# Kernel tuning notes

Measured on AMD Instinct MI355X. Metric: run time of the kernel, lower is better.

Reference implementation:

```python
import jax, jax.numpy as jnp
import numpy as np
from itertools import permutations

S_SPK, B, T, C = 2, 16, 300, 3000
NUM_STATES, NUM_ARCS = 400, 1200
DEN_STATES, DEN_ARCS = 3000, 60000
DEN_SCALE = 1.0
NEG = -1e30


def setup_inputs() -> dict:
    key = jax.random.key(0)
    ks = jax.random.split(key, 14)
    est_llhs = jax.nn.log_softmax(
        jax.random.normal(ks[0], (S_SPK, B, T, C), jnp.float32), axis=-1)
    seqlengths = jax.random.randint(ks[1], (B,), T // 2, T + 1, jnp.int32)
    num_src = jax.random.randint(ks[2], (S_SPK, B, NUM_ARCS), 0, NUM_STATES, jnp.int32)
    num_dst = jax.random.randint(ks[3], (S_SPK, B, NUM_ARCS), 0, NUM_STATES, jnp.int32)
    num_label = jax.random.randint(ks[4], (S_SPK, B, NUM_ARCS), 0, C, jnp.int32)
    num_weight = -2.0 * jax.random.uniform(ks[5], (S_SPK, B, NUM_ARCS), jnp.float32)
    num_start = -5.0 * jax.random.uniform(ks[6], (S_SPK, B, NUM_STATES), jnp.float32)
    num_final = -5.0 * jax.random.uniform(ks[7], (S_SPK, B, NUM_STATES), jnp.float32)
    den_src = jax.random.randint(ks[8], (DEN_ARCS,), 0, DEN_STATES, jnp.int32)
    den_dst = jax.random.randint(ks[9], (DEN_ARCS,), 0, DEN_STATES, jnp.int32)
    den_label = jax.random.randint(ks[10], (DEN_ARCS,), 0, C, jnp.int32)
    den_weight = -2.0 * jax.random.uniform(ks[11], (DEN_ARCS,), jnp.float32)
    den_start = -5.0 * jax.random.uniform(ks[12], (DEN_STATES,), jnp.float32)
    den_final = -5.0 * jax.random.uniform(ks[13], (DEN_STATES,), jnp.float32)
    return dict(est_llhs=est_llhs, seqlengths=seqlengths,
                num_src=num_src, num_dst=num_dst, num_label=num_label,
                num_weight=num_weight, num_start=num_start, num_final=num_final,
                den_src=den_src, den_dst=den_dst, den_label=den_label,
                den_weight=den_weight, den_start=den_start, den_final=den_final)


def _segment_lse(scores, idx, n):
    # stable log-sum-exp scatter over destination states
    m = jax.ops.segment_max(scores, idx, num_segments=n)
    m_safe = jnp.where(jnp.isfinite(m), m, 0.0)
    s = jax.ops.segment_sum(jnp.exp(scores - m_safe[idx]), idx, num_segments=n)
    s_safe = jnp.where(s > 0, s, 1.0)
    return jnp.where(s > 0, m_safe + jnp.log(s_safe), NEG)


def _fsa_logZ(llh, seqlen, src, dst, lab, w, start, final):
    # forward algorithm: alpha_{t+1}[dst] = LSE_arcs(alpha_t[src] + w + llh[t, lab])
    n = start.shape[0]
    mask = jnp.arange(llh.shape[0]) < seqlen

    def step(alpha, inp):
        t_llh, valid = inp
        scores = alpha[src] + w + t_llh[lab]
        new_alpha = _segment_lse(scores, dst, n)
        return jnp.where(valid, new_alpha, alpha), None

    alpha, _ = jax.lax.scan(step, start, (llh, mask))
    return jax.scipy.special.logsumexp(alpha + final)


_num_logZ = jax.vmap(_fsa_logZ)  # all graph args batched over B
_den_logZ = jax.vmap(_fsa_logZ, in_axes=(0, 0, None, None, None, None, None, None))


def reference(est_llhs, seqlengths, num_src, num_dst, num_label, num_weight,
              num_start, num_final, den_src, den_dst, den_label, den_weight,
              den_start, den_final):
    n_spk = est_llhs.shape[0]
    bsz = est_llhs.shape[1]
    # denominator log-marginal per (batch, speaker): [B, S]
    den_llh = jnp.stack(
        [_den_logZ(est_llhs[s], seqlengths, den_src, den_dst, den_label,
                   den_weight, den_start, den_final) for s in range(n_spk)], axis=1)
    # numerator log-marginals for every permutation: [P, B, S]
    perms = list(permutations(range(n_spk)))
    num_llh_perms = jnp.stack([
        jnp.stack([_num_logZ(est_llhs[s], seqlengths, num_src[p], num_dst[p],
                             num_label[p], num_weight[p], num_start[p], num_final[p])
                   for s, p in enumerate(perm)], axis=1)
        for perm in perms], axis=0)
    # best permutation per utterance
    idxs = jnp.argmax(num_llh_perms.sum(axis=2), axis=0)  # [B]
    num_llh = jnp.take_along_axis(
        num_llh_perms, jnp.broadcast_to(idxs[None, :, None], (1, bsz, n_spk)),
        axis=0)[0]  # [B, S]
    loss = -(num_llh - DEN_SCALE * den_llh)
    return loss.sum()
```

## Files before the change

kernel.cpp:

```cpp
#include <hip/hip_runtime.h>
#include <hip/hip_bf16.h>

#define S_SPK 2
#define BATCH 16
#define TMAX 300
#define CLASSES 3000
#define NUM_STATES 400
#define NUM_ARCS 1200
#define DEN_STATES 3000
#define DEN_ARCS 60000

#define BLK 768
#define NWAVE 12
#define KCH 4
#define CHST 750
#define NSEQ 32
#define NUM_CAP_G 2400
#define NGRAPH 32

#define WS_DEN_ARCS   0
#define WS_NUM_ARCS   576000
#define WS_DEN_CNT    1190400
#define WS_DEN_R      1202400
#define WS_DEN_CUR    1214416
#define WS_NUM_CNT    1226416
#define WS_NUM_R      1277616
#define WS_NUM_CUR    1328944
#define WS_GALPHA     1380144
#define WS_FLAGS      2148144
#define WS_BINS       2156336
#define WS_DEN_Z      2156592
#define WS_NUM_Z      2156720
#define WS_BINCUR     2156976
#define WS_PI         2157232
#define WS_INV        2169232
#define WS_CNTP       2181232
#define WS_ZERO_INTS  (2156592 / 4)

__global__ void zero_ws(int* __restrict__ p, int n) {
    int i = blockIdx.x * blockDim.x + threadIdx.x;
    for (; i < n; i += gridDim.x * blockDim.x) p[i] = 0;
}

__global__ void hist_den(const int* __restrict__ dst, int* __restrict__ cnt) {
    int i = blockIdx.x * blockDim.x + threadIdx.x;
    if (i < DEN_ARCS) atomicAdd(&cnt[dst[i]], 1);
}

__global__ void hist_num(const int* __restrict__ dst, int* __restrict__ cnt) {
    int i = blockIdx.x * blockDim.x + threadIdx.x;
    if (i < NGRAPH * NUM_ARCS) {
        int g = i / NUM_ARCS;
        atomicAdd(&cnt[g * NUM_STATES + dst[i]], 1);
    }
}

__global__ void bin_hist(const int* __restrict__ cnt, int* __restrict__ bins) {
    int s = blockIdx.x * blockDim.x + threadIdx.x;
    if (s < DEN_STATES) {
        int c = cnt[s]; if (c > 63) c = 63;
        atomicAdd(&bins[c], 1);
    }
}

__global__ void bin_scan(const int* __restrict__ bins, int* __restrict__ bincur) {
    __shared__ int sb[64];
    int tid = threadIdx.x;
    sb[tid] = bins[tid];
    __syncthreads();
    int sum = 0;
    for (int b = 63; b > tid; --b) sum += sb[b];
    bincur[tid] = sum;
}

__global__ void rank_scatter(const int* __restrict__ cnt, int* __restrict__ bincur,
                             int* __restrict__ pi, int* __restrict__ inv) {
    int s = blockIdx.x * blockDim.x + threadIdx.x;
    if (s < DEN_STATES) {
        int c = cnt[s]; if (c > 63) c = 63;
        int rank = atomicAdd(&bincur[c], 1);
        int pos = (rank & (KCH - 1)) * CHST + (rank >> 2);
        pi[s] = pos;
        inv[pos] = s;
    }
}

__global__ void permute_cnt(const int* __restrict__ cnt, const int* __restrict__ inv,
                            int* __restrict__ cntp) {
    int p = blockIdx.x * blockDim.x + threadIdx.x;
    if (p < DEN_STATES) cntp[p] = cnt[inv[p]];
}

__global__ void scan_den(const int* __restrict__ cnt, int* __restrict__ R) {
    __shared__ int sc[1024];
    int tid = threadIdx.x;
    int c0 = 0, c1 = 0, c2 = 0, p0 = 0, p1 = 0, p2 = 0, pg = 0;
    if (tid < 1000) {
        c0 = cnt[3 * tid]; c1 = cnt[3 * tid + 1]; c2 = cnt[3 * tid + 2];
        p0 = (c0 + 3) & ~3; p1 = (c1 + 3) & ~3; p2 = (c2 + 3) & ~3;
        pg = p0 + p1 + p2;
    }
    sc[tid] = pg; __syncthreads();
    for (int o = 1; o < 1024; o <<= 1) {
        int v = (tid >= o) ? sc[tid - o] : 0;
        __syncthreads(); sc[tid] += v; __syncthreads();
    }
    int ex = sc[tid] - pg;
    if (tid < 1000) {
        R[3 * tid] = ex; R[3 * tid + 1] = ex + p0; R[3 * tid + 2] = ex + p0 + p1;
    }
    if (tid == 1000) R[3000] = ex;
}

__global__ void scan_num(const int* __restrict__ cnt, int* __restrict__ R) {
    __shared__ int sc[512];
    int g = blockIdx.x, tid = threadIdx.x;
    int c = 0, pg = 0;
    if (tid < NUM_STATES) { c = cnt[g * NUM_STATES + tid]; pg = (c + 3) & ~3; }
    sc[tid] = pg; __syncthreads();
    for (int o = 1; o < 512; o <<= 1) {
        int v = (tid >= o) ? sc[tid - o] : 0;
        __syncthreads(); sc[tid] += v; __syncthreads();
    }
    int ex = sc[tid] - pg;
    if (tid <= NUM_STATES) R[g * (NUM_STATES + 1) + tid] = ex;
}

__global__ void scat_den(const int* __restrict__ src, const int* __restrict__ dst,
                         const int* __restrict__ lab, const float* __restrict__ w,
                         const int* __restrict__ R, int* __restrict__ cur,
                         const int* __restrict__ pi, int2* __restrict__ out) {
    int i = blockIdx.x * blockDim.x + threadIdx.x;
    if (i >= DEN_ARCS) return;
    int dpos = pi[dst[i]];
    int spos = pi[src[i]];
    int pos = R[dpos] + atomicAdd(&cur[dpos], 1);
    out[pos] = make_int2(spos | (lab[i] << 16), __float_as_int(__expf(w[i])));
}

__global__ void scat_num(const int* __restrict__ src, const int* __restrict__ dst,
                         const int* __restrict__ lab, const float* __restrict__ w,
                         const int* __restrict__ R, int* __restrict__ cur,
                         int2* __restrict__ out) {
    int i = blockIdx.x * blockDim.x + threadIdx.x;
    if (i >= NGRAPH * NUM_ARCS) return;
    int g = i / NUM_ARCS;
    int d = dst[i];
    int pos = R[g * (NUM_STATES + 1) + d] + atomicAdd(&cur[g * NUM_STATES + d], 1);
    out[g * NUM_CAP_G + pos] =
        make_int2(src[i] | (lab[i] << 16), __float_as_int(__expf(w[i])));
}

__device__ __forceinline__ void num_fwd(
    const int* __restrict__ R, const int2* __restrict__ arcs,
    const float* __restrict__ start, const float* __restrict__ fin,
    const float* __restrict__ est, int L, float* __restrict__ out,
    float* A0, float* A1, float* p, float* red)
{
    const int tid = threadIdx.x, lane = tid & 63, wid = tid >> 6;

    if (tid < NUM_STATES) A0[tid] = __expf(start[tid]);

    int rs = 0, re = 0;
    if (tid < NUM_STATES) { rs = R[tid]; re = R[tid + 1]; }

    float l0 = est[tid], l1 = est[tid + 768], l2 = est[tid + 1536];
    float l3 = (tid < 696) ? est[tid + 2304] : 0.f;

    float c = 1.f, OFF = 0.f, pend = 0.f;
    const int4* arcs4 = (const int4*)arcs;

    for (int t = 0; t < L; ++t) {
        OFF += pend;
        p[tid] = __expf(l0) * c;        p[tid + 768] = __expf(l1) * c;
        p[tid + 1536] = __expf(l2) * c;
        if (tid < 696) p[tid + 2304] = __expf(l3) * c;
        {
            const float* nr = est + (size_t)((t + 1 < L) ? (t + 1) : t) * CLASSES;
            l0 = nr[tid]; l1 = nr[tid + 768]; l2 = nr[tid + 1536];
            if (tid < 696) l3 = nr[tid + 2304];
        }
        __syncthreads();

        const float* Ac = (t & 1) ? A1 : A0;
        float*       An = (t & 1) ? A0 : A1;
        float a0 = 0.f;
        for (int r = rs; r < re; r += 4) {
            int4 q0 = arcs4[(r >> 1)];
            int4 q1 = arcs4[(r >> 1) + 1];
            a0 += Ac[q0.x & 0xffff] * p[((unsigned)q0.x) >> 16] * __int_as_float(q0.y);
            a0 += Ac[q0.z & 0xffff] * p[((unsigned)q0.z) >> 16] * __int_as_float(q0.w);
            a0 += Ac[q1.x & 0xffff] * p[((unsigned)q1.x) >> 16] * __int_as_float(q1.y);
            a0 += Ac[q1.z & 0xffff] * p[((unsigned)q1.z) >> 16] * __int_as_float(q1.w);
        }
        float mymax = 0.f;
        if (tid < NUM_STATES) { An[tid] = a0; mymax = a0; }
        #pragma unroll
        for (int o = 32; o > 0; o >>= 1) mymax = fmaxf(mymax, __shfl_down(mymax, o, 64));
        if (lane == 0) red[wid] = mymax;
        __syncthreads();
        float M = red[0];
        #pragma unroll
        for (int k = 1; k < NWAVE; ++k) M = fmaxf(M, red[k]);
        M = fmaxf(M, 1e-37f);
        c = 1.0f / M;
        pend = __logf(M);
    }

    const float* Af = (L & 1) ? A1 : A0;
    float fs = 0.f;
    if (tid < NUM_STATES) fs = Af[tid] * __expf(fin[tid]);
    __syncthreads();
    #pragma unroll
    for (int o = 32; o > 0; o >>= 1) fs += __shfl_down(fs, o, 64);
    if (lane == 0) red[wid] = fs;
    __syncthreads();
    if (tid == 0) {
        float s = 0.f;
        #pragma unroll
        for (int k = 0; k < NWAVE; ++k) s += red[k];
        out[0] = OFF + __logf(s);
    }
}

__global__ __launch_bounds__(BLK) void forward_kernel(
    const float* __restrict__ est, const int* __restrict__ seqlen,
    const int2* __restrict__ den_arcs, const int* __restrict__ den_R,
    const float* __restrict__ den_start, const float* __restrict__ den_final,
    const int* __restrict__ den_inv,
    const int2* __restrict__ num_arcs, const int* __restrict__ num_R,
    const float* __restrict__ num_start, const float* __restrict__ num_final,
    float* __restrict__ galpha,
    float* __restrict__ den_z, float* __restrict__ num_z)
{
    __shared__ float S1[2][DEN_STATES];
    __shared__ float S2[2][CLASSES];
    __shared__ float red[2][16];

    const int blk = blockIdx.x;
    const int tid = threadIdx.x, lane = tid & 63, wid = tid >> 6;

    if (blk < KCH * NSEQ) {
        const int seq = blk & 31;
        const int chunk = blk >> 5;
        const int b = seq & 15;
        const int L = seqlen[b];
        const float* est_base = est + (size_t)seq * TMAX * CLASSES;
        const int base = chunk * CHST;
        unsigned* gaU = (unsigned*)galpha;

        int rs = 0, re = 0;
        if (tid < CHST) { rs = den_R[base + tid]; re = den_R[base + tid + 1]; }
        const int4* arcs4 = (const int4*)den_arcs;
        const int4* ap = arcs4 + (rs >> 1);
        const int n4 = (re - rs) >> 2;

        float l0 = est_base[tid], l1 = est_base[tid + 768], l2 = est_base[tid + 1536];
        float l3 = (tid < 696) ? est_base[tid + 2304] : 0.f;

        float OFF = 0.f;

        for (int t = 0; t < L; ++t) {
            const int cur = t & 1;
            float* S1c = S1[cur];
            float* S2c = S2[cur];

            S2c[tid] = __expf(l0); S2c[tid + 768] = __expf(l1); S2c[tid + 1536] = __expf(l2);
            if (tid < 696) S2c[tid + 2304] = __expf(l3);
            {
                const float* nr = est_base + (size_t)((t + 1 < L) ? (t + 1) : t) * CLASSES;
                l0 = nr[tid]; l1 = nr[tid + 768]; l2 = nr[tid + 1536];
                if (tid < 696) l3 = nr[tid + 2304];
            }

            int4 a0 = ap[0], a1 = ap[1], b0 = ap[2], b1 = ap[3];

            if (t == 0) {
                S1c[tid]        = __expf(den_start[den_inv[tid]]);
                S1c[tid + 768]  = __expf(den_start[den_inv[tid + 768]]);
                S1c[tid + 1536] = __expf(den_start[den_inv[tid + 1536]]);
                if (tid < 696) S1c[tid + 2304] = __expf(den_start[den_inv[tid + 2304]]);
            } else {
                const unsigned tg = (unsigned)((t - 1) % 3) + 1u;
                const unsigned* gp = gaU + ((size_t)seq * 2 + ((t - 1) & 1)) * DEN_STATES;
                unsigned u0, u1, u2, u3 = tg;
                for (;;) {
                    u0 = __hip_atomic_load(gp + tid,        __ATOMIC_RELAXED, __HIP_MEMORY_SCOPE_AGENT);
                    u1 = __hip_atomic_load(gp + tid + 768,  __ATOMIC_RELAXED, __HIP_MEMORY_SCOPE_AGENT);
                    u2 = __hip_atomic_load(gp + tid + 1536, __ATOMIC_RELAXED, __HIP_MEMORY_SCOPE_AGENT);
                    if (tid < 696)
                        u3 = __hip_atomic_load(gp + tid + 2304, __ATOMIC_RELAXED, __HIP_MEMORY_SCOPE_AGENT);
                    if ((((u0 & 3u) == tg) && ((u1 & 3u) == tg)) &&
                        (((u2 & 3u) == tg) && ((u3 & 3u) == tg))) break;
                    __builtin_amdgcn_s_sleep(1);
                }
                float x0 = __uint_as_float(u0 & ~3u);
                float x1 = __uint_as_float(u1 & ~3u);
                float x2 = __uint_as_float(u2 & ~3u);
                float x3 = (tid < 696) ? __uint_as_float(u3 & ~3u) : 0.f;
                S1c[tid] = x0; S1c[tid + 768] = x1; S1c[tid + 1536] = x2;
                if (tid < 696) S1c[tid + 2304] = x3;
                float mymax = fmaxf(fmaxf(x0, x1), fmaxf(x2, x3));
                #pragma unroll
                for (int o = 32; o > 0; o >>= 1)
                    mymax = fmaxf(mymax, __shfl_down(mymax, o, 64));
                if (lane == 0) red[cur][wid] = mymax;
            }

            __syncthreads();

            float cM = 1.0f;
            if (t) {
                const float4* r4 = (const float4*)red[cur];
                float4 ra = r4[0], rb = r4[1], rc = r4[2];
                float M = fmaxf(fmaxf(fmaxf(ra.x, ra.y), fmaxf(ra.z, ra.w)),
                         fmaxf(fmaxf(fmaxf(rb.x, rb.y), fmaxf(rb.z, rb.w)),
                               fmaxf(fmaxf(rc.x, rc.y), fmaxf(rc.z, rc.w))));
                M = fmaxf(M, 1e-37f);
                cM = 1.0f / M;
                OFF += __logf(M);
            }

            float acc = 0.f;
            for (int i = 0; i < n4; ++i) {
                int4 p0 = ap[2 * i + 4], p1 = ap[2 * i + 5];
                acc += S1c[a0.x & 0xffff] * S2c[((unsigned)a0.x) >> 16] * __int_as_float(a0.y);
                acc += S1c[a0.z & 0xffff] * S2c[((unsigned)a0.z) >> 16] * __int_as_float(a0.w);
                acc += S1c[a1.x & 0xffff] * S2c[((unsigned)a1.x) >> 16] * __int_as_float(a1.y);
                acc += S1c[a1.z & 0xffff] * S2c[((unsigned)a1.z) >> 16] * __int_as_float(a1.w);
                a0 = b0; a1 = b1; b0 = p0; b1 = p1;
            }

            if (tid < CHST) {
                unsigned uv = (__float_as_uint(acc * cM) & ~3u) | ((unsigned)(t % 3) + 1u);
                __hip_atomic_store(gaU + ((size_t)seq * 2 + cur) * DEN_STATES + base + tid,
                                   uv, __ATOMIC_RELAXED, __HIP_MEMORY_SCOPE_AGENT);
            }
            asm volatile("" ::: "memory");
        }

        if (chunk == 0) {
            __syncthreads();
            const unsigned tg = (unsigned)((L - 1) % 3) + 1u;
            const unsigned* gp = gaU + ((size_t)seq * 2 + ((L - 1) & 1)) * DEN_STATES;
            unsigned u0, u1, u2, u3 = tg;
            for (;;) {
                u0 = __hip_atomic_load(gp + tid,        __ATOMIC_RELAXED, __HIP_MEMORY_SCOPE_AGENT);
                u1 = __hip_atomic_load(gp + tid + 768,  __ATOMIC_RELAXED, __HIP_MEMORY_SCOPE_AGENT);
                u2 = __hip_atomic_load(gp + tid + 1536, __ATOMIC_RELAXED, __HIP_MEMORY_SCOPE_AGENT);
                if (tid < 696)
                    u3 = __hip_atomic_load(gp + tid + 2304, __ATOMIC_RELAXED, __HIP_MEMORY_SCOPE_AGENT);
                if ((((u0 & 3u) == tg) && ((u1 & 3u) == tg)) &&
                    (((u2 & 3u) == tg) && ((u3 & 3u) == tg))) break;
                __builtin_amdgcn_s_sleep(1);
            }
            float fs = __uint_as_float(u0 & ~3u) * __expf(den_final[den_inv[tid]])
                     + __uint_as_float(u1 & ~3u) * __expf(den_final[den_inv[tid + 768]])
                     + __uint_as_float(u2 & ~3u) * __expf(den_final[den_inv[tid + 1536]]);
            if (tid < 696)
                fs += __uint_as_float(u3 & ~3u) * __expf(den_final[den_inv[tid + 2304]]);
            #pragma unroll
            for (int o = 32; o > 0; o >>= 1) fs += __shfl_down(fs, o, 64);
            if (lane == 0) red[0][wid] = fs;
            __syncthreads();
            if (tid == 0) {
                float s = 0.f;
                #pragma unroll
                for (int k = 0; k < NWAVE; ++k) s += red[0][k];
                den_z[seq] = OFF + __logf(s);
            }
        }
    } else {
        const int q = blk - KCH * NSEQ;
        const int b = q & 15;
        const int sp = q >> 4;
        const int s = sp >> 1, pp = sp & 1;
        const int L = seqlen[b];
        const int g = pp * BATCH + b;
        num_fwd(num_R + (size_t)g * (NUM_STATES + 1),
                num_arcs + (size_t)g * NUM_CAP_G,
                num_start + (size_t)g * NUM_STATES,
                num_final + (size_t)g * NUM_STATES,
                est + (size_t)(s * BATCH + b) * TMAX * CLASSES, L, &num_z[q],
                &S1[0][0], &S1[0][1536], &S2[0][0], &red[0][0]);
    }
}

__global__ void loss_kernel(const float* __restrict__ den_z,
                            const float* __restrict__ num_z,
                            float* __restrict__ out)
{
    int tid = threadIdx.x;
    float l = 0.f;
    if (tid < BATCH) {
        int b = tid;
        float z00 = num_z[(0 * 2 + 0) * BATCH + b];
        float z01 = num_z[(0 * 2 + 1) * BATCH + b];
        float z10 = num_z[(1 * 2 + 0) * BATCH + b];
        float z11 = num_z[(1 * 2 + 1) * BATCH + b];
        float perm0 = z00 + z11;
        float perm1 = z01 + z10;
        float n0, n1;
        if (perm0 >= perm1) { n0 = z00; n1 = z11; }
        else                { n0 = z01; n1 = z10; }
        l = -(n0 - den_z[0 * BATCH + b]) - (n1 - den_z[1 * BATCH + b]);
    }
    #pragma unroll
    for (int o = 32; o > 0; o >>= 1) l += __shfl_down(l, o, 64);
    if (tid == 0) out[0] = l;
}

extern "C" void kernel_launch(void* const* d_in, const int* in_sizes, int n_in,
                              void* d_out, int out_size, void* d_ws, size_t ws_size,
                              hipStream_t stream) {
    const float* est        = (const float*)d_in[0];
    const int*   seqlen     = (const int*)d_in[1];
    const int*   num_src    = (const int*)d_in[2];
    const int*   num_dst    = (const int*)d_in[3];
    const int*   num_label  = (const int*)d_in[4];
    const float* num_weight = (const float*)d_in[5];
    const float* num_start  = (const float*)d_in[6];
    const float* num_final  = (const float*)d_in[7];
    const int*   den_src    = (const int*)d_in[8];
    const int*   den_dst    = (const int*)d_in[9];
    const int*   den_label  = (const int*)d_in[10];
    const float* den_weight = (const float*)d_in[11];
    const float* den_start  = (const float*)d_in[12];
    const float* den_final  = (const float*)d_in[13];

    char* ws = (char*)d_ws;
    int2*     den_arcs = (int2*)(ws + WS_DEN_ARCS);
    int2*     num_arcs = (int2*)(ws + WS_NUM_ARCS);
    int*      den_cnt  = (int*)(ws + WS_DEN_CNT);
    int*      den_R    = (int*)(ws + WS_DEN_R);
    int*      den_cur  = (int*)(ws + WS_DEN_CUR);
    int*      num_cnt  = (int*)(ws + WS_NUM_CNT);
    int*      num_R    = (int*)(ws + WS_NUM_R);
    int*      num_cur  = (int*)(ws + WS_NUM_CUR);
    float*    galpha   = (float*)(ws + WS_GALPHA);
    int*      bins     = (int*)(ws + WS_BINS);
    float*    den_z    = (float*)(ws + WS_DEN_Z);
    float*    num_z    = (float*)(ws + WS_NUM_Z);
    int*      bincur   = (int*)(ws + WS_BINCUR);
    int*      pi       = (int*)(ws + WS_PI);
    int*      inv      = (int*)(ws + WS_INV);
    int*      cntp     = (int*)(ws + WS_CNTP);

    zero_ws<<<512, 256, 0, stream>>>((int*)ws, WS_ZERO_INTS);
    hist_den<<<(DEN_ARCS + 255) / 256, 256, 0, stream>>>(den_dst, den_cnt);
    hist_num<<<(NGRAPH * NUM_ARCS + 255) / 256, 256, 0, stream>>>(num_dst, num_cnt);

    bin_hist<<<(DEN_STATES + 255) / 256, 256, 0, stream>>>(den_cnt, bins);
    bin_scan<<<1, 64, 0, stream>>>(bins, bincur);
    rank_scatter<<<(DEN_STATES + 255) / 256, 256, 0, stream>>>(den_cnt, bincur, pi, inv);
    permute_cnt<<<(DEN_STATES + 255) / 256, 256, 0, stream>>>(den_cnt, inv, cntp);

    scan_den<<<1, 1024, 0, stream>>>(cntp, den_R);
    scan_num<<<NGRAPH, 512, 0, stream>>>(num_cnt, num_R);
    scat_den<<<(DEN_ARCS + 255) / 256, 256, 0, stream>>>(
        den_src, den_dst, den_label, den_weight, den_R, den_cur, pi, den_arcs);
    scat_num<<<(NGRAPH * NUM_ARCS + 255) / 256, 256, 0, stream>>>(
        num_src, num_dst, num_label, num_weight, num_R, num_cur, num_arcs);

    forward_kernel<<<KCH * NSEQ + S_SPK * S_SPK * BATCH, BLK, 0, stream>>>(
        est, seqlen, den_arcs, den_R, den_start, den_final, inv,
        num_arcs, num_R, num_start, num_final,
        galpha, den_z, num_z);

    loss_kernel<<<1, 64, 0, stream>>>(den_z, num_z, (float*)d_out);
}
```

Measured before the change: 1.602 ms.

## Split denominator across six chunks and merge preprocessing kernels

Raises the number of cooperating blocks per denominator sequence from 4 to 6, with 500 states each, so the forward kernel launches more blocks and gives each block less work per time step. The same change fuses the histogram, binning, ranking, permutation and scan launches into fewer kernels, doing the degree-sorting in shared memory inside one block, which cuts per-launch overhead. The cost is more inter-block synchronisation traffic per time step, and the forward kernel now has to work correctly with the new chunk sizes.

```diff
diff --git a/kernel.cpp b/kernel.cpp
--- a/kernel.cpp
+++ b/kernel.cpp
@@ -12,8 +12,8 @@
 
 #define BLK 768
 #define NWAVE 12
-#define KCH 4
-#define CHST 750
+#define KCH 6
+#define CHST 500
 #define NSEQ 32
 #define NUM_CAP_G 2400
 #define NGRAPH 32
@@ -34,7 +34,6 @@
 #define WS_BINCUR     2156976
 #define WS_PI         2157232
 #define WS_INV        2169232
-#define WS_CNTP       2181232
 #define WS_ZERO_INTS  (2156592 / 4)
 
 __global__ void zero_ws(int* __restrict__ p, int n) {
@@ -42,62 +41,57 @@
     for (; i < n; i += gridDim.x * blockDim.x) p[i] = 0;
 }
 
-__global__ void hist_den(const int* __restrict__ dst, int* __restrict__ cnt) {
+__global__ void hist_all(const int* __restrict__ dden, int* __restrict__ dcnt,
+                         const int* __restrict__ dnum, int* __restrict__ ncnt) {
     int i = blockIdx.x * blockDim.x + threadIdx.x;
-    if (i < DEN_ARCS) atomicAdd(&cnt[dst[i]], 1);
-}
-
-__global__ void hist_num(const int* __restrict__ dst, int* __restrict__ cnt) {
-    int i = blockIdx.x * blockDim.x + threadIdx.x;
+    if (i < DEN_ARCS) atomicAdd(&dcnt[dden[i]], 1);
     if (i < NGRAPH * NUM_ARCS) {
         int g = i / NUM_ARCS;
-        atomicAdd(&cnt[g * NUM_STATES + dst[i]], 1);
-    }
-}
-
-__global__ void bin_hist(const int* __restrict__ cnt, int* __restrict__ bins) {
-    int s = blockIdx.x * blockDim.x + threadIdx.x;
-    if (s < DEN_STATES) {
-        int c = cnt[s]; if (c > 63) c = 63;
-        atomicAdd(&bins[c], 1);
-    }
-}
-
-__global__ void bin_scan(const int* __restrict__ bins, int* __restrict__ bincur) {
-    __shared__ int sb[64];
-    int tid = threadIdx.x;
-    sb[tid] = bins[tid];
-    __syncthreads();
-    int sum = 0;
-    for (int b = 63; b > tid; --b) sum += sb[b];
-    bincur[tid] = sum;
-}
-
-__global__ void rank_scatter(const int* __restrict__ cnt, int* __restrict__ bincur,
-                             int* __restrict__ pi, int* __restrict__ inv) {
-    int s = blockIdx.x * blockDim.x + threadIdx.x;
-    if (s < DEN_STATES) {
-        int c = cnt[s]; if (c > 63) c = 63;
-        int rank = atomicAdd(&bincur[c], 1);
-        int pos = (rank & (KCH - 1)) * CHST + (rank >> 2);
-        pi[s] = pos;
-        inv[pos] = s;
-    }
-}
-
-__global__ void permute_cnt(const int* __restrict__ cnt, const int* __restrict__ inv,
-                            int* __restrict__ cntp) {
-    int p = blockIdx.x * blockDim.x + threadIdx.x;
-    if (p < DEN_STATES) cntp[p] = cnt[inv[p]];
-}
-
-__global__ void scan_den(const int* __restrict__ cnt, int* __restrict__ R) {
-    __shared__ int sc[1024];
-    int tid = threadIdx.x;
-    int c0 = 0, c1 = 0, c2 = 0, p0 = 0, p1 = 0, p2 = 0, pg = 0;
+        atomicAdd(&ncnt[g * NUM_STATES + dnum[i]], 1);
+    }
+}
+
+__global__ void prep_den(const int* __restrict__ cnt, int* __restrict__ pi,
+                         int* __restrict__ inv, int* __restrict__ R) {
+    __shared__ int bins[64], bcur[64], sc[1024];
+    const int tid = threadIdx.x;
+
+    if (tid < 64) bins[tid] = 0;
+    __syncthreads();
+
+    int c0 = 0, c1 = 0, c2 = 0;
     if (tid < 1000) {
         c0 = cnt[3 * tid]; c1 = cnt[3 * tid + 1]; c2 = cnt[3 * tid + 2];
-        p0 = (c0 + 3) & ~3; p1 = (c1 + 3) & ~3; p2 = (c2 + 3) & ~3;
+        atomicAdd(&bins[min(c0, 63)], 1);
+        atomicAdd(&bins[min(c1, 63)], 1);
+        atomicAdd(&bins[min(c2, 63)], 1);
+    }
+    __syncthreads();
+
+    if (tid < 64) {
+        int sum = 0;
+        for (int b = 63; b > tid; --b) sum += bins[b];
+        bcur[tid] = sum;
+    }
+    __syncthreads();
+
+    if (tid < 1000) {
+        int cc[3] = { c0, c1, c2 };
+        #pragma unroll
+        for (int j = 0; j < 3; ++j) {
+            int c = min(cc[j], 63);
+            int rank = atomicAdd(&bcur[c], 1);
+            int pos = (rank % KCH) * CHST + rank / KCH;
+            pi[3 * tid + j] = pos;
+            inv[pos] = 3 * tid + j;
+        }
+    }
+    __syncthreads();
+
+    int d0 = 0, d1 = 0, d2 = 0, p0 = 0, p1 = 0, p2 = 0, pg = 0;
+    if (tid < 1000) {
+        d0 = cnt[inv[3 * tid]]; d1 = cnt[inv[3 * tid + 1]]; d2 = cnt[inv[3 * tid + 2]];
+        p0 = (d0 + 3) & ~3; p1 = (d1 + 3) & ~3; p2 = (d2 + 3) & ~3;
         pg = p0 + p1 + p2;
     }
     sc[tid] = pg; __syncthreads();
@@ -126,29 +120,29 @@
     if (tid <= NUM_STATES) R[g * (NUM_STATES + 1) + tid] = ex;
 }
 
-__global__ void scat_den(const int* __restrict__ src, const int* __restrict__ dst,
-                         const int* __restrict__ lab, const float* __restrict__ w,
-                         const int* __restrict__ R, int* __restrict__ cur,
-                         const int* __restrict__ pi, int2* __restrict__ out) {
+__global__ void scat_all(
+    const int* __restrict__ dsrc, const int* __restrict__ ddst,
+    const int* __restrict__ dlab, const float* __restrict__ dw,
+    const int* __restrict__ dR, int* __restrict__ dcur,
+    const int* __restrict__ pi, int2* __restrict__ dout,
+    const int* __restrict__ nsrc, const int* __restrict__ ndst,
+    const int* __restrict__ nlab, const float* __restrict__ nw,
+    const int* __restrict__ nR, int* __restrict__ ncur, int2* __restrict__ nout)
+{
     int i = blockIdx.x * blockDim.x + threadIdx.x;
-    if (i >= DEN_ARCS) return;
-    int dpos = pi[dst[i]];
-    int spos = pi[src[i]];
-    int pos = R[dpos] + atomicAdd(&cur[dpos], 1);
-    out[pos] = make_int2(spos | (lab[i] << 16), __float_as_int(__expf(w[i])));
-}
-
-__global__ void scat_num(const int* __restrict__ src, const int* __restrict__ dst,
-                         const int* __restrict__ lab, const float* __restrict__ w,
-                         const int* __restrict__ R, int* __restrict__ cur,
-                         int2* __restrict__ out) {
-    int i = blockIdx.x * blockDim.x + threadIdx.x;
-    if (i >= NGRAPH * NUM_ARCS) return;
-    int g = i / NUM_ARCS;
-    int d = dst[i];
-    int pos = R[g * (NUM_STATES + 1) + d] + atomicAdd(&cur[g * NUM_STATES + d], 1);
-    out[g * NUM_CAP_G + pos] =
-        make_int2(src[i] | (lab[i] << 16), __float_as_int(__expf(w[i])));
+    if (i < DEN_ARCS) {
+        int dpos = pi[ddst[i]];
+        int spos = pi[dsrc[i]];
+        int pos = dR[dpos] + atomicAdd(&dcur[dpos], 1);
+        dout[pos] = make_int2(spos | (dlab[i] << 16), __float_as_int(__expf(dw[i])));
+    }
+    if (i < NGRAPH * NUM_ARCS) {
+        int g = i / NUM_ARCS;
+        int d = ndst[i];
+        int pos = nR[g * (NUM_STATES + 1) + d] + atomicAdd(&ncur[g * NUM_STATES + d], 1);
+        nout[g * NUM_CAP_G + pos] =
+            make_int2(nsrc[i] | (nlab[i] << 16), __float_as_int(__expf(nw[i])));
+    }
 }
 
 __device__ __forceinline__ void num_fwd(
@@ -438,28 +432,18 @@
     int*      num_R    = (int*)(ws + WS_NUM_R);
     int*      num_cur  = (int*)(ws + WS_NUM_CUR);
     float*    galpha   = (float*)(ws + WS_GALPHA);
-    int*      bins     = (int*)(ws + WS_BINS);
     float*    den_z    = (float*)(ws + WS_DEN_Z);
     float*    num_z    = (float*)(ws + WS_NUM_Z);
-    int*      bincur   = (int*)(ws + WS_BINCUR);
     int*      pi       = (int*)(ws + WS_PI);
     int*      inv      = (int*)(ws + WS_INV);
-    int*      cntp     = (int*)(ws + WS_CNTP);
 
     zero_ws<<<512, 256, 0, stream>>>((int*)ws, WS_ZERO_INTS);
-    hist_den<<<(DEN_ARCS + 255) / 256, 256, 0, stream>>>(den_dst, den_cnt);
-    hist_num<<<(NGRAPH * NUM_ARCS + 255) / 256, 256, 0, stream>>>(num_dst, num_cnt);
-
-    bin_hist<<<(DEN_STATES + 255) / 256, 256, 0, stream>>>(den_cnt, bins);
-    bin_scan<<<1, 64, 0, stream>>>(bins, bincur);
-    rank_scatter<<<(DEN_STATES + 255) / 256, 256, 0, stream>>>(den_cnt, bincur, pi, inv);
-    permute_cnt<<<(DEN_STATES + 255) / 256, 256, 0, stream>>>(den_cnt, inv, cntp);
-
-    scan_den<<<1, 1024, 0, stream>>>(cntp, den_R);
+    hist_all<<<(DEN_ARCS + 255) / 256, 256, 0, stream>>>(den_dst, den_cnt,
+                                                         num_dst, num_cnt);
+    prep_den<<<1, 1024, 0, stream>>>(den_cnt, pi, inv, den_R);
     scan_num<<<NGRAPH, 512, 0, stream>>>(num_cnt, num_R);
-    scat_den<<<(DEN_ARCS + 255) / 256, 256, 0, stream>>>(
-        den_src, den_dst, den_label, den_weight, den_R, den_cur, pi, den_arcs);
-    scat_num<<<(NGRAPH * NUM_ARCS + 255) / 256, 256, 0, stream>>>(
+    scat_all<<<(DEN_ARCS + 255) / 256, 256, 0, stream>>>(
+        den_src, den_dst, den_label, den_weight, den_R, den_cur, pi, den_arcs,
         num_src, num_dst, num_label, num_weight, num_R, num_cur, num_arcs);
 
     forward_kernel<<<KCH * NSEQ + S_SPK * S_SPK * BATCH, BLK, 0, stream>>>(
```

After: 1.563 ms. -2.5%, faster.
